# Performance work log

Hardware: AMD Instinct MI355X
Metric: run time of the kernel (lower is better)

## Reference

```python
import jax, jax.numpy as jnp
import numpy as np

B, T, H = 8, 2048, 2048

def glorot(key, shape):
    return jax.random.uniform(key, shape, minval=-1.0, maxval=1.0) * jnp.sqrt(2 / sum(shape))

def setup_inputs() -> dict:
    key = jax.random.key(0)
    kx, kr, ka, kb = jax.random.split(key, 4)
    x_seq = jax.random.normal(kx, (B, T, H), dtype=jnp.float32)
    reset = jax.random.randint(kr, (B, T), 0, 2).astype(bool)
    a_mat = glorot(ka, (H, H))
    b_mat = glorot(kb, (H, H))
    return {"x_seq": x_seq, "reset": reset, "a_mat": a_mat, "b_mat": b_mat}

def reference(x_seq, reset, a_mat, b_mat):
    # Precompute B^T x_t for all timesteps in one big GEMM: (B^T x)_k = sum_h b[h,k] x[h]
    bx = jnp.einsum('hk,bth->btk', b_mat, x_seq)  # [B,T,H]
    bx_t = jnp.swapaxes(bx, 0, 1)                 # [T,B,H] time-major
    reset_t = jnp.swapaxes(reset, 0, 1)           # [T,B]

    def step(h, inp):
        bx_step, r = inp                          # [B,H], [B]
        h = jnp.where(r[:, None], 0.0, h)         # reset hidden state
        h = h @ a_mat.T + bx_step                 # A @ h per batch row
        return h, h

    h0 = jnp.zeros((B, H), dtype=x_seq.dtype)
    _, h_seq = jax.lax.scan(step, h0, (bx_t, reset_t))
    return jnp.swapaxes(h_seq, 0, 1)              # [B,T,H]
```

## Files before the change

kernel.cpp:

```cpp
#include <hip/hip_runtime.h>

#define Hn 2048
#define Bn 8
#define Tn 2048
#define Cn 16
#define NCn (Tn / Cn)
#define M2n (NCn * Bn)

using f32x4 = __attribute__((ext_vector_type(4))) float;
using u32x4 = __attribute__((ext_vector_type(4))) unsigned int;
using us4   = __attribute__((ext_vector_type(4))) unsigned short;
using bf8   = __attribute__((ext_vector_type(8))) short;
using f4    = __attribute__((ext_vector_type(4))) float;

#define GLOAD16(g, l) __builtin_amdgcn_global_load_lds(                      \
    (const __attribute__((address_space(1))) void*)(g),                      \
    (__attribute__((address_space(3))) void*)(l), 16, 0, 0)

__device__ __forceinline__ unsigned short f2bf(float f) {
    unsigned u = __builtin_bit_cast(unsigned, f);
    u = u + 0x7fffu + ((u >> 16) & 1u);
    return (unsigned short)(u >> 16);
}
__device__ __forceinline__ float bf2f(unsigned short h) {
    unsigned u = ((unsigned)h) << 16;
    return __builtin_bit_cast(float, u);
}
__device__ __forceinline__ void split2f(float v, unsigned short& a, unsigned short& b) {
    a = f2bf(v);
    b = f2bf(v - bf2f(a));
}

__global__ __launch_bounds__(256) void k_reset_prep(const unsigned int* __restrict__ rin,
                                                    unsigned char* __restrict__ r8,
                                                    int* __restrict__ cut,
                                                    int* __restrict__ firstReset,
                                                    int* __restrict__ anyUncut,
                                                    int* __restrict__ perm,
                                                    int* __restrict__ iperm,
                                                    int* __restrict__ counts) {
    __shared__ int s_badInt, s_badFloat;
    __shared__ int hist[17], off[18], cur[17];
    if (threadIdx.x == 0) { s_badInt = 0; s_badFloat = 0; *anyUncut = 0; }
    if (threadIdx.x < 17) hist[threadIdx.x] = 0;
    __syncthreads();
    int badI = 0, badF = 0;
    for (int i = threadIdx.x; i < 4096; i += 256) {
        unsigned int v = rin[i];
        if (v > 1u) badI = 1;
        if (v != 0u && v != 0x3f800000u) badF = 1;
    }
    if (badI) atomicOr(&s_badInt, 1);
    if (badF) atomicOr(&s_badFloat, 1);
    __syncthreads();
    const int fmt = (!s_badInt) ? 0 : ((!s_badFloat) ? 1 : 2);
    const unsigned char* rb = (const unsigned char*)rin;
    const float* rf = (const float*)rin;
    for (int i = threadIdx.x; i < Bn * Tn; i += 256) {
        unsigned char v;
        if (fmt == 0)      v = (unsigned char)(rin[i] != 0u);
        else if (fmt == 1) v = (unsigned char)(rf[i] != 0.0f);
        else               v = (unsigned char)(rb[i] != 0);
        r8[i] = v;
    }
    __syncthreads();
    int anyU = 0;
    for (int m = threadIdx.x; m < M2n; m += 256) {
        int c = m / Bn, b = m % Bn;
        int fr = Cn;
        for (int j = 0; j < Cn; j++) {
            if (r8[b * Tn + c * Cn + j]) { fr = j; break; }
        }
        firstReset[m] = fr;
        int ct = (fr < Cn);
        cut[m] = ct;
        if (!ct && c < NCn - 1) anyU = 1;
        atomicAdd(&hist[fr], 1);
    }
    if (anyU) atomicOr(anyUncut, 1);
    __syncthreads();
    if (threadIdx.x == 0) {
        off[16] = 0;
        for (int v = 15; v >= 0; v--) off[v] = off[v + 1] + hist[v + 1];
        for (int v = 0; v < 17; v++) cur[v] = (v == 16) ? 0 : off[v];
        for (int j = 0; j < 16; j++) counts[j] = off[j];
    }
    __syncthreads();
    for (int m = threadIdx.x; m < M2n; m += 256) {
        int fr = firstReset[m];
        int pos = atomicAdd(&cur[fr], 1);
        perm[pos] = m;
        iperm[m] = pos;
    }
}

__global__ __launch_bounds__(256) void k_split_A2(const float* __restrict__ A,
                                                  unsigned short* __restrict__ a1,
                                                  unsigned short* __restrict__ a2) {
    size_t i = ((size_t)blockIdx.x * 256 + threadIdx.x) * 4;
    f32x4 v = *(const f32x4*)&A[i];
    us4 h1, h2;
#pragma unroll
    for (int e = 0; e < 4; e++) {
        unsigned short x1, x2;
        split2f(v[e], x1, x2);
        h1[e] = x1; h2[e] = x2;
    }
    *(us4*)&a1[i] = h1; *(us4*)&a2[i] = h2;
}

__global__ __launch_bounds__(256) void k_split_Bt(const float* __restrict__ Bm,
                                                  unsigned short* __restrict__ b1,
                                                  unsigned short* __restrict__ b2) {
    __shared__ float tile[64][65];
    const int k0 = blockIdx.y * 64, n0 = blockIdx.x * 64;
    const int c = threadIdx.x & 63, r4 = threadIdx.x >> 6;
#pragma unroll
    for (int i = 0; i < 16; i++) {
        int r = r4 * 16 + i;
        tile[r][c] = Bm[(size_t)(k0 + r) * Hn + n0 + c];
    }
    __syncthreads();
#pragma unroll
    for (int i = 0; i < 16; i++) {
        int r = r4 * 16 + i;
        float v = tile[c][r];
        unsigned short x1, x2;
        split2f(v, x1, x2);
        b1[(size_t)(n0 + r) * Hn + k0 + c] = x1;
        b2[(size_t)(n0 + r) * Hn + k0 + c] = x2;
    }
}

__global__ __launch_bounds__(256) void k_split_X(const float* __restrict__ X,
                                                 unsigned short* __restrict__ x1,
                                                 unsigned short* __restrict__ x2) {
    size_t i = ((size_t)blockIdx.x * 256 + threadIdx.x) * 4;
    f32x4 v = *(const f32x4*)&X[i];
    us4 h1, h2;
#pragma unroll
    for (int e = 0; e < 4; e++) {
        unsigned short a, b;
        split2f(v[e], a, b);
        h1[e] = a; h2[e] = b;
    }
    *(us4*)&x1[i] = h1; *(us4*)&x2[i] = h2;
}

template<int PREX>
__global__ __launch_bounds__(512) void k_gemm_p1(const unsigned short* __restrict__ X0,
                                                 const unsigned short* __restrict__ X1,
                                                 const unsigned short* __restrict__ B0,
                                                 const unsigned short* __restrict__ B1,
                                                 const float* __restrict__ Xf,
                                                 float* __restrict__ Out,
                                                 unsigned short* __restrict__ S0,
                                                 unsigned short* __restrict__ S1) {
    constexpr int BM = 256, BN = 128, LW = 32;
    __shared__ unsigned short ldsA[2 * BM * LW];
    __shared__ unsigned short ldsB[2 * BN * LW];
    const int tid = threadIdx.x;
    const int lane = tid & 63;
    const int wv = tid >> 6;
    const int wm = wv >> 1, wn = wv & 1;
    const int n0 = blockIdx.x * BN;
    const int m0 = blockIdx.y * BM;

    f4 acc[4][4];
#pragma unroll
    for (int fm = 0; fm < 4; fm++)
#pragma unroll
        for (int fn = 0; fn < 4; fn++) acc[fm][fn] = (f4){0.f, 0.f, 0.f, 0.f};

    const unsigned short* gA[4];
    unsigned short* lA[4];
    const float* gX[2];
    unsigned short* lX[2];
    const unsigned short* gB[2];
    unsigned short* lB[2];
    if constexpr (PREX) {
#pragma unroll
        for (int q = 0; q < 4; q++) {
            int u = tid + q * 512;
            int sp = u >> 10, row = (u >> 2) & 255, slot = u & 3;
            int g = slot ^ ((row >> 1) & 3);
            gA[q] = (sp ? X1 : X0) + (size_t)(m0 + row) * Hn + g * 8;
            lA[q] = &ldsA[u * 8];
        }
    } else {
#pragma unroll
        for (int q = 0; q < 2; q++) {
            int u = tid + q * 512;
            int row = u >> 2, slot = u & 3;
            int s = slot ^ ((row >> 1) & 3);
            gX[q] = Xf + (size_t)(m0 + row) * Hn + slot * 8;
            lX[q] = &ldsA[row * LW + s * 8];
        }
    }
#pragma unroll
    for (int q = 0; q < 2; q++) {
        int u = tid + q * 512;
        int sp = u >> 9, row = (u >> 2) & 127, slot = u & 3;
        int g = slot ^ ((row >> 1) & 3);
        gB[q] = (sp ? B1 : B0) + (size_t)(n0 + row) * Hn + g * 8;
        lB[q] = &ldsB[u * 8];
    }
    const int sl = (lane >> 4) ^ ((lane >> 1) & 3);
    const int pa[3] = {0, 0, 1};
    const int pb[3] = {0, 1, 0};

    if constexpr (PREX) {
#pragma unroll
        for (int q = 0; q < 4; q++) { GLOAD16(gA[q], lA[q]); gA[q] += 32; }
#pragma unroll
        for (int q = 0; q < 2; q++) { GLOAD16(gB[q], lB[q]); gB[q] += 32; }

        for (int k0 = 0; k0 < Hn; k0 += 32) {
            asm volatile("s_waitcnt vmcnt(0)" ::: "memory");
            __builtin_amdgcn_sched_barrier(0);
            __builtin_amdgcn_s_barrier();

            bf8 af[2][4], bfr[2][4];
#pragma unroll
            for (int sp = 0; sp < 2; sp++)
#pragma unroll
                for (int f = 0; f < 4; f++)
                    af[sp][f] = *(const bf8*)&ldsA[(sp * BM + wm * 64 + f * 16 + (lane & 15)) * LW + sl * 8];
#pragma unroll
            for (int sp = 0; sp < 2; sp++)
#pragma unroll
                for (int f = 0; f < 4; f++)
                    bfr[sp][f] = *(const bf8*)&ldsB[(sp * BN + wn * 64 + f * 16 + (lane & 15)) * LW + sl * 8];
            asm volatile("s_waitcnt lgkmcnt(0)" ::: "memory");
            __builtin_amdgcn_sched_barrier(0);
            __builtin_amdgcn_s_barrier();

            if (k0 + 32 < Hn) {
#pragma unroll
                for (int q = 0; q < 4; q++) { GLOAD16(gA[q], lA[q]); gA[q] += 32; }
#pragma unroll
                for (int q = 0; q < 2; q++) { GLOAD16(gB[q], lB[q]); gB[q] += 32; }
            }
            __builtin_amdgcn_sched_barrier(0);

#pragma unroll
            for (int p = 0; p < 3; p++)
#pragma unroll
                for (int fm = 0; fm < 4; fm++)
#pragma unroll
                    for (int fn = 0; fn < 4; fn++)
                        acc[fm][fn] = __builtin_amdgcn_mfma_f32_16x16x32_bf16(
                            af[pa[p]][fm], bfr[pb[p]][fn], acc[fm][fn], 0, 0, 0);
        }
    } else {
        for (int k0 = 0; k0 < Hn; k0 += 32) {
#pragma unroll
            for (int q = 0; q < 2; q++) {
                f32x4 va = *(const f32x4*)gX[q];
                f32x4 vb = *(const f32x4*)(gX[q] + 4);
                gX[q] += 32;
                us4 h1a, h2a, h1b, h2b;
#pragma unroll
                for (int e = 0; e < 4; e++) {
                    unsigned short p, r;
                    split2f(va[e], p, r); h1a[e] = p; h2a[e] = r;
                    split2f(vb[e], p, r); h1b[e] = p; h2b[e] = r;
                }
                *(us4*)lX[q] = h1a;
                *(us4*)(lX[q] + 4) = h1b;
                *(us4*)(lX[q] + BM * LW) = h2a;
                *(us4*)(lX[q] + BM * LW + 4) = h2b;
            }
#pragma unroll
            for (int q = 0; q < 2; q++) {
                GLOAD16(gB[q], lB[q]);
                gB[q] += 32;
            }
            __syncthreads();

            bf8 af[2][4], bfr[2][4];
#pragma unroll
            for (int sp = 0; sp < 2; sp++)
#pragma unroll
                for (int f = 0; f < 4; f++)
                    af[sp][f] = *(const bf8*)&ldsA[(sp * BM + wm * 64 + f * 16 + (lane & 15)) * LW + sl * 8];
#pragma unroll
            for (int sp = 0; sp < 2; sp++)
#pragma unroll
                for (int f = 0; f < 4; f++)
                    bfr[sp][f] = *(const bf8*)&ldsB[(sp * BN + wn * 64 + f * 16 + (lane & 15)) * LW + sl * 8];
#pragma unroll
            for (int p = 0; p < 3; p++)
#pragma unroll
                for (int fm = 0; fm < 4; fm++)
#pragma unroll
                    for (int fn = 0; fn < 4; fn++)
                        acc[fm][fn] = __builtin_amdgcn_mfma_f32_16x16x32_bf16(
                            af[pa[p]][fm], bfr[pb[p]][fn], acc[fm][fn], 0, 0, 0);
            __syncthreads();
        }
    }

#pragma unroll
    for (int fm = 0; fm < 4; fm++)
#pragma unroll
        for (int r = 0; r < 4; r++) {
            int row = m0 + wm * 64 + fm * 16 + (lane >> 4) * 4 + r;
            int bb = row >> 11, t = row & 2047;
            int isC0 = ((t & 15) == 0);
            size_t ob = (size_t)row * Hn;
            size_t sb = (size_t)((t >> 4) * 8 + bb) * Hn;
#pragma unroll
            for (int fn = 0; fn < 4; fn++) {
                int n = n0 + wn * 64 + fn * 16 + (lane & 15);
                float v = acc[fm][fn][r];
                Out[ob + n] = v;
                if (isC0) {
                    unsigned short h1, h2;
                    split2f(v, h1, h2);
                    S0[sb + n] = h1; S1[sb + n] = h2;
                }
            }
        }
}

template<int PHASE>
__global__ __launch_bounds__(256) void k_gemm_s(const unsigned short* __restrict__ S0,
                                                const unsigned short* __restrict__ S1,
                                                const unsigned short* __restrict__ W0,
                                                const unsigned short* __restrict__ W1,
                                                float* __restrict__ Out,
                                                unsigned short* __restrict__ O0,
                                                unsigned short* __restrict__ O1,
                                                const unsigned char* __restrict__ r8v,
                                                const int* __restrict__ perm,
                                                const int* __restrict__ iperm,
                                                const int* __restrict__ counts,
                                                unsigned short* __restrict__ U0,
                                                unsigned short* __restrict__ U1,
                                                float* __restrict__ Hin,
                                                int j) {
    constexpr int BM = 64, BN = 64, BK = 64;
    constexpr int TSZ = 2 * BM * BK;
    constexpr int NT = Hn / BK;
    __shared__ unsigned short ldsA[2 * TSZ];
    __shared__ unsigned short ldsB[2 * TSZ];
    const int tid = threadIdx.x;
    const int lane = tid & 63;
    const int wv = tid >> 6;
    const int wm = wv >> 1, wn = wv & 1;
    const int n0 = blockIdx.x * BN;
    const int m0 = blockIdx.y * BM;

    int cnt = 0;
    if constexpr (PHASE == 4) {
        cnt = counts[j];
        if (m0 >= cnt) return;
    }

    f4 acc[2][2];
#pragma unroll
    for (int fm = 0; fm < 2; fm++)
#pragma unroll
        for (int fn = 0; fn < 2; fn++) acc[fm][fn] = (f4){0.f, 0.f, 0.f, 0.f};

    const unsigned short* gA[4];
    unsigned short* lA[4];
    const unsigned short* gB[4];
    unsigned short* lB[4];
#pragma unroll
    for (int q = 0; q < 4; q++) {
        int u = tid + q * 256;
        int sp = u >> 9, row = (u >> 3) & 63, s = u & 7;
        int g = s ^ (row & 7);
        gA[q] = (sp ? S1 : S0) + (size_t)(m0 + row) * Hn + g * 8;
        lA[q] = &ldsA[u * 8];
        gB[q] = (sp ? W1 : W0) + (size_t)(n0 + row) * Hn + g * 8;
        lB[q] = &ldsB[u * 8];
    }
    const int pa[3] = {0, 0, 1};
    const int pb[3] = {0, 1, 0};

#define STAGE_S(bsel)                                                        \
    {                                                                        \
        const int boff_ = (bsel) * TSZ;                                      \
        _Pragma("unroll")                                                    \
        for (int q = 0; q < 4; q++) {                                        \
            GLOAD16(gA[q], lA[q] + boff_);                                   \
            GLOAD16(gB[q], lB[q] + boff_);                                   \
            gA[q] += BK; gB[q] += BK;                                        \
        }                                                                    \
    }

    STAGE_S(0);
    STAGE_S(1);

    for (int t = 0; t < NT; t++) {
        if (t == NT - 1) { asm volatile("s_waitcnt vmcnt(0)" ::: "memory"); }
        else             { asm volatile("s_waitcnt vmcnt(8)" ::: "memory"); }
        __builtin_amdgcn_sched_barrier(0);
        __builtin_amdgcn_s_barrier();

        const unsigned short* curA = &ldsA[(t & 1) * TSZ];
        const unsigned short* curB = &ldsB[(t & 1) * TSZ];
        bf8 af[2][2][2], bfr[2][2][2];
#pragma unroll
        for (int h = 0; h < 2; h++) {
            const int slh = ((h * 4) + (lane >> 4)) ^ (lane & 7);
#pragma unroll
            for (int sp = 0; sp < 2; sp++)
#pragma unroll
                for (int f = 0; f < 2; f++) {
                    af[h][sp][f] = *(const bf8*)&curA[(sp * BM + wm * 32 + f * 16 + (lane & 15)) * BK + slh * 8];
                    bfr[h][sp][f] = *(const bf8*)&curB[(sp * BN + wn * 32 + f * 16 + (lane & 15)) * BK + slh * 8];
                }
        }
        asm volatile("s_waitcnt lgkmcnt(0)" ::: "memory");
        __builtin_amdgcn_sched_barrier(0);
        __builtin_amdgcn_s_barrier();

        if (t + 2 < NT) STAGE_S(t & 1);
        __builtin_amdgcn_sched_barrier(0);

#pragma unroll
        for (int h = 0; h < 2; h++)
#pragma unroll
            for (int p = 0; p < 3; p++)
#pragma unroll
                for (int fm = 0; fm < 2; fm++)
#pragma unroll
                    for (int fn = 0; fn < 2; fn++)
                        acc[fm][fn] = __builtin_amdgcn_mfma_f32_16x16x32_bf16(
                            af[h][pa[p]][fm], bfr[h][pb[p]][fn], acc[fm][fn], 0, 0, 0);
    }
#undef STAGE_S

    if constexpr (PHASE == 2 || PHASE == 3) {
#pragma unroll
        for (int fm = 0; fm < 2; fm++)
#pragma unroll
            for (int r = 0; r < 4; r++) {
                int m = m0 + wm * 32 + fm * 16 + (lane >> 4) * 4 + r;
                int cch = m >> 3, bb = m & 7;
                int t = cch * Cn + j;
                int rfl = r8v[bb * Tn + t];
                size_t ob = ((size_t)bb * Tn + t) * (size_t)Hn;
                size_t sb = (size_t)m * Hn;
                int carry = 0;
                size_t ub = 0, hb = 0;
                if constexpr (PHASE == 3) {
                    carry = (m < M2n - 8);
                    if (carry) {
                        ub = (size_t)iperm[m + 8] * Hn;
                        hb = (size_t)(m + 8) * Hn;
                    }
                }
#pragma unroll
                for (int fn = 0; fn < 2; fn++) {
                    int n = n0 + wn * 32 + fn * 16 + (lane & 15);
                    float v = (rfl ? 0.0f : acc[fm][fn][r]) + Out[ob + n];
                    Out[ob + n] = v;
                    unsigned short h1, h2;
                    split2f(v, h1, h2);
                    O0[sb + n] = h1; O1[sb + n] = h2;
                    if constexpr (PHASE == 3) {
                        if (carry) {
                            U0[ub + n] = h1; U1[ub + n] = h2;
                            Hin[hb + n] = v;
                        }
                    }
                }
            }
    } else {
#pragma unroll
        for (int fm = 0; fm < 2; fm++)
#pragma unroll
            for (int r = 0; r < 4; r++) {
                int s = m0 + wm * 32 + fm * 16 + (lane >> 4) * 4 + r;
                int alive = (s < cnt);
                int m = perm[s];
                int cch = m >> 3, bb = m & 7;
                int t = cch * Cn + j;
                size_t ob = ((size_t)bb * Tn + t) * (size_t)Hn;
                size_t sb = (size_t)s * Hn;
#pragma unroll
                for (int fn = 0; fn < 2; fn++) {
                    int n = n0 + wn * 32 + fn * 16 + (lane & 15);
                    if (alive) {
                        float val = acc[fm][fn][r];
                        unsigned short h1, h2;
                        split2f(val, h1, h2);
                        O0[sb + n] = h1; O1[sb + n] = h2;
                        Out[ob + n] += val;
                    }
                }
            }
    }
}

__global__ __launch_bounds__(256) void k_zero_c0(const int* __restrict__ iperm,
                                                 unsigned short* __restrict__ U0,
                                                 unsigned short* __restrict__ U1,
                                                 float* __restrict__ Hin) {
    int b = blockIdx.x;
    int s = iperm[b];
    for (int n = threadIdx.x; n < Hn; n += 256) {
        U0[(size_t)s * Hn + n] = 0;
        U1[(size_t)s * Hn + n] = 0;
        Hin[(size_t)b * Hn + n] = 0.0f;
    }
}

__global__ __launch_bounds__(1024) void k_fallback(float* __restrict__ Hin,
                                                   const float* __restrict__ A,
                                                   const int* __restrict__ cut,
                                                   const int* __restrict__ anyUncut,
                                                   unsigned short* __restrict__ u1,
                                                   unsigned short* __restrict__ u2,
                                                   const int* __restrict__ iperm) {
    if (*anyUncut == 0) return;
    __shared__ float v0[Hn];
    __shared__ float v1[Hn];
    for (int c = 1; c < NCn; c++) {
        for (int b = 0; b < Bn; b++) {
            if (cut[(c - 1) * Bn + b]) continue;
            for (int n = threadIdx.x; n < Hn; n += 1024)
                v0[n] = Hin[((size_t)(c - 1) * Bn + b) * Hn + n];
            __syncthreads();
            for (int s = 0; s < Cn; s++) {
                float* pin = (s & 1) ? v1 : v0;
                float* pout = (s & 1) ? v0 : v1;
                for (int n = threadIdx.x; n < Hn; n += 1024) {
                    float accv = 0.0f;
                    const float* Ar = &A[(size_t)n * Hn];
                    for (int k = 0; k < Hn; k++) accv += pin[k] * Ar[k];
                    pout[n] = accv;
                }
                __syncthreads();
            }
            float* pres = (Cn & 1) ? v1 : v0;
            int mrow = c * Bn + b;
            size_t dst = (size_t)mrow * Hn;
            size_t sdst = (size_t)iperm[mrow] * Hn;
            for (int n = threadIdx.x; n < Hn; n += 1024) {
                float nv = Hin[dst + n] + pres[n];
                Hin[dst + n] = nv;
                unsigned short h1, h2;
                split2f(nv, h1, h2);
                u1[sdst + n] = h1; u2[sdst + n] = h2;
            }
            __syncthreads();
        }
    }
}

extern "C" void kernel_launch(void* const* d_in, const int* in_sizes, int n_in,
                              void* d_out, int out_size, void* d_ws, size_t ws_size,
                              hipStream_t stream) {
    const float* x = (const float*)d_in[0];
    const unsigned int* rst = (const unsigned int*)d_in[1];
    const float* Am = (const float*)d_in[2];
    const float* Bm = (const float*)d_in[3];
    float* Out = (float*)d_out;
    char* ws = (char*)d_ws;

    unsigned char* r8 = (unsigned char*)ws;
    int* cut = (int*)(ws + 16384);
    int* firstReset = (int*)(ws + 20480);
    int* perm = (int*)(ws + 24576);
    int* iperm = (int*)(ws + 28672);
    int* counts = (int*)(ws + 32768);
    int* anyUncut = (int*)(ws + 32832);
    unsigned short* a1 = (unsigned short*)(ws + 65536);
    unsigned short* a2 = a1 + 4194304;
    unsigned short* b1 = a2 + 4194304;
    unsigned short* b2 = b1 + 4194304;
    unsigned short* sP1 = b2 + 4194304;
    unsigned short* sP2 = sP1 + 2097152;
    unsigned short* sQ1 = sP2 + 2097152;
    unsigned short* sQ2 = sQ1 + 2097152;
    unsigned short* uP1 = sQ2 + 2097152;
    unsigned short* uP2 = uP1 + 2097152;
    float* Hin = (float*)(uP2 + 2097152);
    unsigned short* x1 = (unsigned short*)(Hin + 2097152);
    unsigned short* x2 = x1 + 33554432;
    const size_t NEED_X = 201392128ull;
    const bool prex = (ws_size >= NEED_X);

    k_reset_prep<<<1, 256, 0, stream>>>(rst, r8, cut, firstReset, anyUncut, perm, iperm, counts);
    k_split_A2<<<4096, 256, 0, stream>>>(Am, a1, a2);
    k_split_Bt<<<dim3(32, 32), 256, 0, stream>>>(Bm, b1, b2);

    if (prex) {
        k_split_X<<<32768, 256, 0, stream>>>(x, x1, x2);
        k_gemm_p1<1><<<dim3(Hn / 128, (Bn * Tn) / 256), 512, 0, stream>>>(
            x1, x2, b1, b2, nullptr, Out, sP1, sP2);
    } else {
        k_gemm_p1<0><<<dim3(Hn / 128, (Bn * Tn) / 256), 512, 0, stream>>>(
            nullptr, nullptr, b1, b2, x, Out, sP1, sP2);
    }

    for (int j = 1; j < Cn; j++) {
        const unsigned short* i1 = (j & 1) ? sP1 : sQ1;
        const unsigned short* i2 = (j & 1) ? sP2 : sQ2;
        unsigned short* o1 = (j & 1) ? sQ1 : sP1;
        unsigned short* o2 = (j & 1) ? sQ2 : sP2;
        if (j < Cn - 1) {
            k_gemm_s<2><<<dim3(Hn / 64, M2n / 64), 256, 0, stream>>>(
                i1, i2, a1, a2, Out, o1, o2, r8, nullptr, nullptr, nullptr,
                nullptr, nullptr, nullptr, j);
        } else {
            k_gemm_s<3><<<dim3(Hn / 64, M2n / 64), 256, 0, stream>>>(
                i1, i2, a1, a2, Out, o1, o2, r8, nullptr, iperm, nullptr,
                uP1, uP2, Hin, j);
        }
    }

    k_zero_c0<<<8, 256, 0, stream>>>(iperm, uP1, uP2, Hin);
    k_fallback<<<1, 1024, 0, stream>>>(Hin, Am, cut, anyUncut, uP1, uP2, iperm);

    for (int j = 0; j < Cn; j++) {
        const unsigned short* i1 = (j == 0) ? uP1 : ((j & 1) ? sP1 : sQ1);
        const unsigned short* i2 = (j == 0) ? uP2 : ((j & 1) ? sP2 : sQ2);
        unsigned short* o1 = (j & 1) ? sQ1 : sP1;
        unsigned short* o2 = (j & 1) ? sQ2 : sP2;
        k_gemm_s<4><<<dim3(Hn / 64, M2n / 64), 256, 0, stream>>>(
            i1, i2, a1, a2, Out, o1, o2, nullptr, perm, nullptr, counts,
            nullptr, nullptr, nullptr, j);
    }
}
```

Baseline: 1.288 ms.

## Merge prep kernels, fold zeroing into gemm, simplify p1 loop, add setprio

Combines the reset prep, A/B/X split kernels into one launch with block-index dispatch, and folds the chunk-0 zeroing kernel into the last k_gemm_s epilogue, removing several kernel launches. The prex GEMM path loses its software-pipelined prefetch (loads issued before compute of the previous tile) and now uses the simple load-sync-compute loop. The diff also adds s_setprio around the MFMA block in k_gemm_s. Dropping the prefetch may expose global latency in the big GEMM, and the folded zeroing relies on correct ordering against the writes in the same epilogue.

```diff
diff --git a/kernel.cpp b/kernel.cpp
--- a/kernel.cpp
+++ b/kernel.cpp
@@ -31,120 +31,127 @@
     b = f2bf(v - bf2f(a));
 }
 
-__global__ __launch_bounds__(256) void k_reset_prep(const unsigned int* __restrict__ rin,
-                                                    unsigned char* __restrict__ r8,
-                                                    int* __restrict__ cut,
-                                                    int* __restrict__ firstReset,
-                                                    int* __restrict__ anyUncut,
-                                                    int* __restrict__ perm,
-                                                    int* __restrict__ iperm,
-                                                    int* __restrict__ counts) {
-    __shared__ int s_badInt, s_badFloat;
-    __shared__ int hist[17], off[18], cur[17];
-    if (threadIdx.x == 0) { s_badInt = 0; s_badFloat = 0; *anyUncut = 0; }
-    if (threadIdx.x < 17) hist[threadIdx.x] = 0;
-    __syncthreads();
-    int badI = 0, badF = 0;
-    for (int i = threadIdx.x; i < 4096; i += 256) {
-        unsigned int v = rin[i];
-        if (v > 1u) badI = 1;
-        if (v != 0u && v != 0x3f800000u) badF = 1;
-    }
-    if (badI) atomicOr(&s_badInt, 1);
-    if (badF) atomicOr(&s_badFloat, 1);
-    __syncthreads();
-    const int fmt = (!s_badInt) ? 0 : ((!s_badFloat) ? 1 : 2);
-    const unsigned char* rb = (const unsigned char*)rin;
-    const float* rf = (const float*)rin;
-    for (int i = threadIdx.x; i < Bn * Tn; i += 256) {
-        unsigned char v;
-        if (fmt == 0)      v = (unsigned char)(rin[i] != 0u);
-        else if (fmt == 1) v = (unsigned char)(rf[i] != 0.0f);
-        else               v = (unsigned char)(rb[i] != 0);
-        r8[i] = v;
-    }
-    __syncthreads();
-    int anyU = 0;
-    for (int m = threadIdx.x; m < M2n; m += 256) {
-        int c = m / Bn, b = m % Bn;
-        int fr = Cn;
-        for (int j = 0; j < Cn; j++) {
-            if (r8[b * Tn + c * Cn + j]) { fr = j; break; }
-        }
-        firstReset[m] = fr;
-        int ct = (fr < Cn);
-        cut[m] = ct;
-        if (!ct && c < NCn - 1) anyU = 1;
-        atomicAdd(&hist[fr], 1);
-    }
-    if (anyU) atomicOr(anyUncut, 1);
-    __syncthreads();
-    if (threadIdx.x == 0) {
-        off[16] = 0;
-        for (int v = 15; v >= 0; v--) off[v] = off[v + 1] + hist[v + 1];
-        for (int v = 0; v < 17; v++) cur[v] = (v == 16) ? 0 : off[v];
-        for (int j = 0; j < 16; j++) counts[j] = off[j];
-    }
-    __syncthreads();
-    for (int m = threadIdx.x; m < M2n; m += 256) {
-        int fr = firstReset[m];
-        int pos = atomicAdd(&cur[fr], 1);
-        perm[pos] = m;
-        iperm[m] = pos;
-    }
-}
-
-__global__ __launch_bounds__(256) void k_split_A2(const float* __restrict__ A,
-                                                  unsigned short* __restrict__ a1,
-                                                  unsigned short* __restrict__ a2) {
-    size_t i = ((size_t)blockIdx.x * 256 + threadIdx.x) * 4;
-    f32x4 v = *(const f32x4*)&A[i];
-    us4 h1, h2;
-#pragma unroll
-    for (int e = 0; e < 4; e++) {
-        unsigned short x1, x2;
-        split2f(v[e], x1, x2);
-        h1[e] = x1; h2[e] = x2;
-    }
-    *(us4*)&a1[i] = h1; *(us4*)&a2[i] = h2;
-}
-
-__global__ __launch_bounds__(256) void k_split_Bt(const float* __restrict__ Bm,
-                                                  unsigned short* __restrict__ b1,
-                                                  unsigned short* __restrict__ b2) {
-    __shared__ float tile[64][65];
-    const int k0 = blockIdx.y * 64, n0 = blockIdx.x * 64;
-    const int c = threadIdx.x & 63, r4 = threadIdx.x >> 6;
-#pragma unroll
-    for (int i = 0; i < 16; i++) {
-        int r = r4 * 16 + i;
-        tile[r][c] = Bm[(size_t)(k0 + r) * Hn + n0 + c];
-    }
-    __syncthreads();
-#pragma unroll
-    for (int i = 0; i < 16; i++) {
-        int r = r4 * 16 + i;
-        float v = tile[c][r];
-        unsigned short x1, x2;
-        split2f(v, x1, x2);
-        b1[(size_t)(n0 + r) * Hn + k0 + c] = x1;
-        b2[(size_t)(n0 + r) * Hn + k0 + c] = x2;
-    }
-}
-
-__global__ __launch_bounds__(256) void k_split_X(const float* __restrict__ X,
-                                                 unsigned short* __restrict__ x1,
-                                                 unsigned short* __restrict__ x2) {
-    size_t i = ((size_t)blockIdx.x * 256 + threadIdx.x) * 4;
-    f32x4 v = *(const f32x4*)&X[i];
-    us4 h1, h2;
-#pragma unroll
-    for (int e = 0; e < 4; e++) {
-        unsigned short a, b;
-        split2f(v[e], a, b);
-        h1[e] = a; h2[e] = b;
-    }
-    *(us4*)&x1[i] = h1; *(us4*)&x2[i] = h2;
+__global__ __launch_bounds__(256) void k_prep(const float* __restrict__ A,
+                                              unsigned short* __restrict__ a1,
+                                              unsigned short* __restrict__ a2,
+                                              const float* __restrict__ Bm,
+                                              unsigned short* __restrict__ b1,
+                                              unsigned short* __restrict__ b2,
+                                              const float* __restrict__ X,
+                                              unsigned short* __restrict__ x1,
+                                              unsigned short* __restrict__ x2,
+                                              const unsigned int* __restrict__ rin,
+                                              unsigned char* __restrict__ r8,
+                                              int* __restrict__ cut,
+                                              int* __restrict__ firstReset,
+                                              int* __restrict__ anyUncut,
+                                              int* __restrict__ perm,
+                                              int* __restrict__ iperm,
+                                              int* __restrict__ counts) {
+    const int bid = blockIdx.x;
+    if (bid < 4096) {
+        size_t i = ((size_t)bid * 256 + threadIdx.x) * 4;
+        f32x4 v = *(const f32x4*)&A[i];
+        us4 h1, h2;
+#pragma unroll
+        for (int e = 0; e < 4; e++) {
+            unsigned short p, r;
+            split2f(v[e], p, r);
+            h1[e] = p; h2[e] = r;
+        }
+        *(us4*)&a1[i] = h1; *(us4*)&a2[i] = h2;
+        return;
+    }
+    if (bid < 5120) {
+        __shared__ float tile[64][65];
+        int t = bid - 4096;
+        const int k0 = (t >> 5) * 64, n0 = (t & 31) * 64;
+        const int c = threadIdx.x & 63, r4 = threadIdx.x >> 6;
+#pragma unroll
+        for (int i = 0; i < 16; i++) {
+            int r = r4 * 16 + i;
+            tile[r][c] = Bm[(size_t)(k0 + r) * Hn + n0 + c];
+        }
+        __syncthreads();
+#pragma unroll
+        for (int i = 0; i < 16; i++) {
+            int r = r4 * 16 + i;
+            float v = tile[c][r];
+            unsigned short p, q;
+            split2f(v, p, q);
+            b1[(size_t)(n0 + r) * Hn + k0 + c] = p;
+            b2[(size_t)(n0 + r) * Hn + k0 + c] = q;
+        }
+        return;
+    }
+    if (bid == 5120) {
+        __shared__ int s_badInt, s_badFloat;
+        __shared__ int hist[17], off[18], cur[17];
+        if (threadIdx.x == 0) { s_badInt = 0; s_badFloat = 0; *anyUncut = 0; }
+        if (threadIdx.x < 17) hist[threadIdx.x] = 0;
+        __syncthreads();
+        int badI = 0, badF = 0;
+        for (int i = threadIdx.x; i < 4096; i += 256) {
+            unsigned int v = rin[i];
+            if (v > 1u) badI = 1;
+            if (v != 0u && v != 0x3f800000u) badF = 1;
+        }
+        if (badI) atomicOr(&s_badInt, 1);
+        if (badF) atomicOr(&s_badFloat, 1);
+        __syncthreads();
+        const int fmt = (!s_badInt) ? 0 : ((!s_badFloat) ? 1 : 2);
+        const unsigned char* rb = (const unsigned char*)rin;
+        const float* rf = (const float*)rin;
+        for (int i = threadIdx.x; i < Bn * Tn; i += 256) {
+            unsigned char v;
+            if (fmt == 0)      v = (unsigned char)(rin[i] != 0u);
+            else if (fmt == 1) v = (unsigned char)(rf[i] != 0.0f);
+            else               v = (unsigned char)(rb[i] != 0);
+            r8[i] = v;
+        }
+        __syncthreads();
+        int anyU = 0;
+        for (int m = threadIdx.x; m < M2n; m += 256) {
+            int c = m / Bn, b = m % Bn;
+            int fr = Cn;
+            for (int j = 0; j < Cn; j++) {
+                if (r8[b * Tn + c * Cn + j]) { fr = j; break; }
+            }
+            firstReset[m] = fr;
+            int ct = (fr < Cn);
+            cut[m] = ct;
+            if (!ct && c < NCn - 1) anyU = 1;
+            atomicAdd(&hist[fr], 1);
+        }
+        if (anyU) atomicOr(anyUncut, 1);
+        __syncthreads();
+        if (threadIdx.x == 0) {
+            off[16] = 0;
+            for (int v = 15; v >= 0; v--) off[v] = off[v + 1] + hist[v + 1];
+            for (int v = 0; v < 17; v++) cur[v] = (v == 16) ? 0 : off[v];
+            for (int j = 0; j < 16; j++) counts[j] = off[j];
+        }
+        __syncthreads();
+        for (int m = threadIdx.x; m < M2n; m += 256) {
+            int fr = firstReset[m];
+            int pos = atomicAdd(&cur[fr], 1);
+            perm[pos] = m;
+            iperm[m] = pos;
+        }
+        return;
+    }
+    {
+        size_t i = ((size_t)(bid - 5121) * 256 + threadIdx.x) * 4;
+        f32x4 v = *(const f32x4*)&X[i];
+        us4 h1, h2;
+#pragma unroll
+        for (int e = 0; e < 4; e++) {
+            unsigned short p, r;
+            split2f(v[e], p, r);
+            h1[e] = p; h2[e] = r;
+        }
+        *(us4*)&x1[i] = h1; *(us4*)&x2[i] = h2;
+    }
 }
 
 template<int PREX>
@@ -209,51 +216,14 @@
     const int pa[3] = {0, 0, 1};
     const int pb[3] = {0, 1, 0};
 
-    if constexpr (PREX) {
-#pragma unroll
-        for (int q = 0; q < 4; q++) { GLOAD16(gA[q], lA[q]); gA[q] += 32; }
-#pragma unroll
-        for (int q = 0; q < 2; q++) { GLOAD16(gB[q], lB[q]); gB[q] += 32; }
-
-        for (int k0 = 0; k0 < Hn; k0 += 32) {
-            asm volatile("s_waitcnt vmcnt(0)" ::: "memory");
-            __builtin_amdgcn_sched_barrier(0);
-            __builtin_amdgcn_s_barrier();
-
-            bf8 af[2][4], bfr[2][4];
-#pragma unroll
-            for (int sp = 0; sp < 2; sp++)
-#pragma unroll
-                for (int f = 0; f < 4; f++)
-                    af[sp][f] = *(const bf8*)&ldsA[(sp * BM + wm * 64 + f * 16 + (lane & 15)) * LW + sl * 8];
-#pragma unroll
-            for (int sp = 0; sp < 2; sp++)
-#pragma unroll
-                for (int f = 0; f < 4; f++)
-                    bfr[sp][f] = *(const bf8*)&ldsB[(sp * BN + wn * 64 + f * 16 + (lane & 15)) * LW + sl * 8];
-            asm volatile("s_waitcnt lgkmcnt(0)" ::: "memory");
-            __builtin_amdgcn_sched_barrier(0);
-            __builtin_amdgcn_s_barrier();
-
-            if (k0 + 32 < Hn) {
-#pragma unroll
-                for (int q = 0; q < 4; q++) { GLOAD16(gA[q], lA[q]); gA[q] += 32; }
-#pragma unroll
-                for (int q = 0; q < 2; q++) { GLOAD16(gB[q], lB[q]); gB[q] += 32; }
-            }
-            __builtin_amdgcn_sched_barrier(0);
-
-#pragma unroll
-            for (int p = 0; p < 3; p++)
-#pragma unroll
-                for (int fm = 0; fm < 4; fm++)
-#pragma unroll
-                    for (int fn = 0; fn < 4; fn++)
-                        acc[fm][fn] = __builtin_amdgcn_mfma_f32_16x16x32_bf16(
-                            af[pa[p]][fm], bfr[pb[p]][fn], acc[fm][fn], 0, 0, 0);
-        }
-    } else {
-        for (int k0 = 0; k0 < Hn; k0 += 32) {
+    for (int k0 = 0; k0 < Hn; k0 += 32) {
+        if constexpr (PREX) {
+#pragma unroll
+            for (int q = 0; q < 4; q++) {
+                GLOAD16(gA[q], lA[q]);
+                gA[q] += 32;
+            }
+        } else {
 #pragma unroll
             for (int q = 0; q < 2; q++) {
                 f32x4 va = *(const f32x4*)gX[q];
@@ -271,34 +241,35 @@
                 *(us4*)(lX[q] + BM * LW) = h2a;
                 *(us4*)(lX[q] + BM * LW + 4) = h2b;
             }
-#pragma unroll
-            for (int q = 0; q < 2; q++) {
-                GLOAD16(gB[q], lB[q]);
-                gB[q] += 32;
-            }
-            __syncthreads();
-
-            bf8 af[2][4], bfr[2][4];
-#pragma unroll
-            for (int sp = 0; sp < 2; sp++)
-#pragma unroll
-                for (int f = 0; f < 4; f++)
-                    af[sp][f] = *(const bf8*)&ldsA[(sp * BM + wm * 64 + f * 16 + (lane & 15)) * LW + sl * 8];
-#pragma unroll
-            for (int sp = 0; sp < 2; sp++)
-#pragma unroll
-                for (int f = 0; f < 4; f++)
-                    bfr[sp][f] = *(const bf8*)&ldsB[(sp * BN + wn * 64 + f * 16 + (lane & 15)) * LW + sl * 8];
-#pragma unroll
-            for (int p = 0; p < 3; p++)
-#pragma unroll
-                for (int fm = 0; fm < 4; fm++)
-#pragma unroll
-                    for (int fn = 0; fn < 4; fn++)
-                        acc[fm][fn] = __builtin_amdgcn_mfma_f32_16x16x32_bf16(
-                            af[pa[p]][fm], bfr[pb[p]][fn], acc[fm][fn], 0, 0, 0);
-            __syncthreads();
-        }
+        }
+#pragma unroll
+        for (int q = 0; q < 2; q++) {
+            GLOAD16(gB[q], lB[q]);
+            gB[q] += 32;
+        }
+        __syncthreads();
+
+        bf8 af[2][4], bfr[2][4];
+#pragma unroll
+        for (int sp = 0; sp < 2; sp++)
+#pragma unroll
+            for (int f = 0; f < 4; f++)
+                af[sp][f] = *(const bf8*)&ldsA[(sp * BM + wm * 64 + f * 16 + (lane & 15)) * LW + sl * 8];
+#pragma unroll
+        for (int sp = 0; sp < 2; sp++)
+#pragma unroll
+            for (int f = 0; f < 4; f++)
+                bfr[sp][f] = *(const bf8*)&ldsB[(sp * BN + wn * 64 + f * 16 + (lane & 15)) * LW + sl * 8];
+
+#pragma unroll
+        for (int p = 0; p < 3; p++)
+#pragma unroll
+            for (int fm = 0; fm < 4; fm++)
+#pragma unroll
+                for (int fn = 0; fn < 4; fn++)
+                    acc[fm][fn] = __builtin_amdgcn_mfma_f32_16x16x32_bf16(
+                        af[pa[p]][fm], bfr[pb[p]][fn], acc[fm][fn], 0, 0, 0);
+        __syncthreads();
     }
 
 #pragma unroll
@@ -422,6 +393,7 @@
         if (t + 2 < NT) STAGE_S(t & 1);
         __builtin_amdgcn_sched_barrier(0);
 
+        __builtin_amdgcn_s_setprio(1);
 #pragma unroll
         for (int h = 0; h < 2; h++)
 #pragma unroll
@@ -432,6 +404,7 @@
                     for (int fn = 0; fn < 2; fn++)
                         acc[fm][fn] = __builtin_amdgcn_mfma_f32_16x16x32_bf16(
                             af[h][pa[p]][fm], bfr[h][pb[p]][fn], acc[fm][fn], 0, 0, 0);
+        __builtin_amdgcn_s_setprio(0);
     }
 #undef STAGE_S
 
@@ -468,6 +441,11 @@
                             U0[ub + n] = h1; U1[ub + n] = h2;
                             Hin[hb + n] = v;
                         }
+                        if (m < 8) {
+                            size_t zb = (size_t)iperm[m] * Hn;
+                            U0[zb + n] = 0; U1[zb + n] = 0;
+                            Hin[(size_t)m * Hn + n] = 0.0f;
+                        }
                     }
                 }
             }
@@ -495,19 +473,6 @@
                     }
                 }
             }
-    }
-}
-
-__global__ __launch_bounds__(256) void k_zero_c0(const int* __restrict__ iperm,
-                                                 unsigned short* __restrict__ U0,
-                                                 unsigned short* __restrict__ U1,
-                                                 float* __restrict__ Hin) {
-    int b = blockIdx.x;
-    int s = iperm[b];
-    for (int n = threadIdx.x; n < Hn; n += 256) {
-        U0[(size_t)s * Hn + n] = 0;
-        U1[(size_t)s * Hn + n] = 0;
-        Hin[(size_t)b * Hn + n] = 0.0f;
     }
 }
 
@@ -587,12 +552,12 @@
     const size_t NEED_X = 201392128ull;
     const bool prex = (ws_size >= NEED_X);
 
-    k_reset_prep<<<1, 256, 0, stream>>>(rst, r8, cut, firstReset, anyUncut, perm, iperm, counts);
-    k_split_A2<<<4096, 256, 0, stream>>>(Am, a1, a2);
-    k_split_Bt<<<dim3(32, 32), 256, 0, stream>>>(Bm, b1, b2);
+    int prep_grid = prex ? (5121 + 32768) : 5121;
+    k_prep<<<prep_grid, 256, 0, stream>>>(Am, a1, a2, Bm, b1, b2,
+                                          x, x1, x2, rst, r8, cut, firstReset,
+                                          anyUncut, perm, iperm, counts);
 
     if (prex) {
-        k_split_X<<<32768, 256, 0, stream>>>(x, x1, x2);
         k_gemm_p1<1><<<dim3(Hn / 128, (Bn * Tn) / 256), 512, 0, stream>>>(
             x1, x2, b1, b2, nullptr, Out, sP1, sP2);
     } else {
@@ -616,7 +581,6 @@
         }
     }
 
-    k_zero_c0<<<8, 256, 0, stream>>>(iperm, uP1, uP2, Hin);
     k_fallback<<<1, 1024, 0, stream>>>(Hin, Am, cut, anyUncut, uP1, uP2, iperm);
 
     for (int j = 0; j < Cn; j++) {
```

After: 1.235 ms, median of 2. 1.04x faster.
